# Optimization experiments

Hardware: AMD Instinct MI355X
Metric: run time of the kernel (lower is better)

Reference implementation:

```python
import jax, jax.numpy as jnp
import numpy as np

EPS = 1e-7


def setup_inputs() -> dict:
    key = jax.random.key(0)
    kx, kw, kv, kp = jax.random.split(key, 4)
    B, H, Wd, d, V, O = 4, 64, 64, 64, 64, 64
    X = jax.random.normal(kx, (B, H, Wd, d), dtype=jnp.float32)
    W = jax.random.normal(kw, (d, V), dtype=jnp.float32)
    # positive variances (kmeans-style init in original); avoid near-zero divisors
    variance = jax.random.uniform(kv, (d, V), dtype=jnp.float32) + 0.5
    weight = jax.random.normal(kp, (d, O), dtype=jnp.float32) * (1.0 / np.sqrt(d))
    return {"X": X, "W": W, "variance": variance, "weight": weight}


def reference(X, W, variance, weight):
    B, H, Wd, d = X.shape
    V = W.shape[1]
    HW = H * Wd
    Xf = X.reshape(B, HW, d)
    # Faithful replication of torch code: extend = tile(X, V) over last axis,
    # then reshape (d*V) -> (d, V) with k = a*V + c, so the X component at
    # grid position (a, c) is X[..., (a*V + c) % d].
    idx = (jnp.arange(d)[:, None] * V + jnp.arange(V)[None, :]) % d  # (d, V)
    Xg = Xf[:, :, idx]                      # (B, HW, d, V)
    q1 = (Xg - W) / variance                # (B, HW, d, V), broadcast (d,V)
    q = jnp.sum(q1 * q1, axis=2)            # (B, HW, V) squared Mahalanobis-ish dist
    q = q - jnp.min(q, axis=-1, keepdims=True)
    Q = jnp.exp(-0.5 * q)
    Q = Q / jnp.sum(Q, axis=-1, keepdims=True)          # soft assignment (B, HW, V)
    # Raw row-major reinterpretation (B, HW, d*V) -> (B, d, HW, V), as in torch
    z = q1.reshape(B, d, HW, V)
    zQ = z * Q[:, None, :, :]                            # (B, d, HW, V)
    z = jnp.sum(zQ, axis=2)                              # (B, d, V)
    Qsum = jnp.sum(Q, axis=1)                            # (B, V)
    z = (z + EPS) / (Qsum[:, None, :] + EPS)
    norm = jnp.sum(z * z, axis=1, keepdims=True)         # (B, 1, V)
    Z = z / norm                                          # (B, d, V)
    Adj = jnp.einsum('bdv,bdu->bvu', Z, Z)               # (B, V, V)
    out = jnp.einsum('bdv,do->bvo', Z, weight)           # (B, V, O)
    out = jnp.einsum('bvu,buo->bvo', Adj, out)           # (B, V, O)
    Zo = jax.nn.relu(out)
    Xn = jnp.einsum('bnv,bvo->bno', Q, Zo)               # (B, HW, O)
    return Xn.reshape(B, H, Wd, -1).transpose(0, 3, 1, 2)  # (B, O, H, W)
```

## Files before the change

### kernel.cpp

```cpp
#include <hip/hip_runtime.h>

#define HW 4096
#define EPSF 1e-7f

#define WS_S1  0
#define WS_S2P 16384
#define WS_QSP 32768
#define WS_Z   49152
#define WS_ZO  65536
#define WS_Q   81920

__global__ __launch_bounds__(512) void kA(const float* __restrict__ X,
                                          const float* __restrict__ Wm,
                                          const float* __restrict__ var,
                                          float* __restrict__ ws) {
    int b = blockIdx.x >> 6, l = blockIdx.x & 63;
    int w8 = threadIdx.x >> 6, j = threadIdx.x & 63;
    __shared__ float red[3][8][64];
    __shared__ float abc[3][64];
    float invr[8], wivr[8];
    float a = 0.f, bq = 0.f, c = 0.f;
#pragma unroll
    for (int k = 0; k < 8; k++) {
        int i = w8 * 8 + k;
        float v  = var[i * 64 + j];
        float wv = Wm[i * 64 + j];
        float iv = 1.0f / v;
        invr[k] = iv; wivr[k] = wv * iv;
        float iv2 = iv * iv;
        a += iv2; bq += wv * iv2; c += wv * wv * iv2;
    }
    red[0][w8][j] = a; red[1][w8][j] = bq; red[2][w8][j] = c;
    __syncthreads();
    if (threadIdx.x < 64) {
        float t0 = 0.f, t1 = 0.f, t2 = 0.f;
#pragma unroll
        for (int t = 0; t < 8; t++) { t0 += red[0][t][j]; t1 += red[1][t][j]; t2 += red[2][t][j]; }
        abc[0][j] = t0; abc[1][j] = t1; abc[2][j] = t2;
    }
    __syncthreads();
    float Aj = abc[0][j], Bj = abc[1][j], Cj = abc[2][j];

    float s1 = 0.f, s2 = 0.f, qsum = 0.f;
#pragma unroll
    for (int k = 0; k < 8; k++) {
        int i = w8 * 8 + k;
        int n = l * 64 + i;
        float x = X[((b * HW) + n) * 64 + j];
        float q = fmaf(fmaf(Aj, x, -2.0f * Bj), x, Cj);
        float m = q;
        for (int off = 1; off < 64; off <<= 1) m = fminf(m, __shfl_xor(m, off));
        float e = __expf(-0.5f * (q - m));
        float s = e;
        for (int off = 1; off < 64; off <<= 1) s += __shfl_xor(s, off);
        float Qv = e / s;
        ws[WS_Q + ((size_t)(b * HW) + n) * 64 + j] = Qv;
        s1 = fmaf(invr[k], Qv, s1);
        s2 = fmaf(wivr[k], Qv, s2);
        qsum += Qv;
    }
    __syncthreads();
    red[0][w8][j] = s1; red[1][w8][j] = s2; red[2][w8][j] = qsum;
    __syncthreads();
    if (threadIdx.x < 64) {
        float t0 = 0.f, t1 = 0.f, t2 = 0.f;
#pragma unroll
        for (int t = 0; t < 8; t++) { t0 += red[0][t][j]; t1 += red[1][t][j]; t2 += red[2][t][j]; }
        int idx = (b * 64 + l) * 64 + j;
        ws[WS_S1  + idx] = t0;
        ws[WS_S2P + idx] = t1;
        ws[WS_QSP + idx] = t2;
    }
}

__global__ __launch_bounds__(512) void kB(const float* __restrict__ X,
                                          float* __restrict__ ws) {
    int b = blockIdx.x >> 6, h = blockIdx.x & 63;
    int w8 = threadIdx.x >> 6, j = threadIdx.x & 63;
    float acc = 0.f, ps2 = 0.f, pqs = 0.f;
#pragma unroll
    for (int k = 0; k < 8; k++) {
        int l = w8 * 8 + k;
        float x = X[((size_t)(b * HW) + h * 64 + l) * 64 + j];
        int idx = (b * 64 + l) * 64 + j;
        acc = fmaf(x, ws[WS_S1 + idx], acc);
        ps2 += ws[WS_S2P + idx];
        pqs += ws[WS_QSP + idx];
    }
    __shared__ float ra[8][64], rb[8][64], rc[8][64];
    ra[w8][j] = acc; rb[w8][j] = ps2; rc[w8][j] = pqs;
    __syncthreads();
    if (threadIdx.x < 64) {
        float a = 0.f, s2 = 0.f, qs = 0.f;
#pragma unroll
        for (int t = 0; t < 8; t++) { a += ra[t][j]; s2 += rb[t][j]; qs += rc[t][j]; }
        ws[WS_Z + (b * 64 + h) * 64 + j] = (a - s2 + EPSF) / (qs + EPSF);
    }
}

__global__ __launch_bounds__(512) void kCD(const float* __restrict__ weight,
                                           float* __restrict__ ws) {
    int b = blockIdx.x >> 6, v = blockIdx.x & 63;
    int w8 = threadIdx.x >> 6, j = threadIdx.x & 63;
    __shared__ float zl[64][65];
    __shared__ float wl[64][65];
    __shared__ float red[8][64];
    __shared__ float sN[64], sin2[64], ghat[64], yv[64];
#pragma unroll
    for (int k = 0; k < 8; k++) {
        int idx = threadIdx.x + 512 * k;
        int r = idx >> 6, cc = idx & 63;
        zl[r][cc] = ws[WS_Z + b * 4096 + idx];
        wl[r][cc] = weight[idx];
    }
    __syncthreads();
    {
        float na = 0.f;
#pragma unroll
        for (int k = 0; k < 8; k++) { float zz = zl[w8 * 8 + k][j]; na = fmaf(zz, zz, na); }
        red[w8][j] = na;
        __syncthreads();
        if (threadIdx.x < 64) {
            float s = 0.f;
#pragma unroll
            for (int t = 0; t < 8; t++) s += red[t][j];
            sN[j] = s; sin2[j] = 1.0f / (s * s);
        }
        __syncthreads();
    }
    {
        float g = 0.f;
#pragma unroll
        for (int k = 0; k < 8; k++) { int d = w8 * 8 + k; g = fmaf(zl[d][v], zl[d][j], g); }
        red[w8][j] = g;
        __syncthreads();
        if (threadIdx.x < 64) {
            float s = 0.f;
#pragma unroll
            for (int t = 0; t < 8; t++) s += red[t][j];
            ghat[j] = s * sin2[j];
        }
        __syncthreads();
    }
    {
        float y = 0.f;
#pragma unroll
        for (int k = 0; k < 8; k++) { int u = w8 * 8 + k; y = fmaf(ghat[u], zl[j][u], y); }
        red[w8][j] = y;
        __syncthreads();
        if (threadIdx.x < 64) {
            float s = 0.f;
#pragma unroll
            for (int t = 0; t < 8; t++) s += red[t][j];
            yv[j] = s;
        }
        __syncthreads();
    }
    {
        float a = 0.f;
#pragma unroll
        for (int k = 0; k < 8; k++) { int d = w8 * 8 + k; a = fmaf(yv[d], wl[d][j], a); }
        red[w8][j] = a;
        __syncthreads();
        if (threadIdx.x < 64) {
            float s = 0.f;
#pragma unroll
            for (int t = 0; t < 8; t++) s += red[t][j];
            float r = s / sN[v];
            r = r > 0.f ? r : 0.f;
            ws[WS_ZO + (b * 64 + v) * 64 + j] = r;
        }
    }
}

__global__ __launch_bounds__(512) void kF(const float* __restrict__ ws,
                                          float* __restrict__ out) {
    int b = blockIdx.x >> 6, tb = blockIdx.x & 63;
    int nbase = tb * 64;
    int w8 = threadIdx.x >> 6, lane = threadIdx.x & 63;
    int o8 = w8 * 8;
    __shared__ float qs[64][65];
    __shared__ float zo[64][68];
#pragma unroll
    for (int k = 0; k < 8; k++) {
        int idx = threadIdx.x + 512 * k;
        int r = idx >> 6, cc = idx & 63;
        qs[r][cc] = ws[WS_Q + ((size_t)(b * HW) + nbase + r) * 64 + cc];
        zo[r][cc] = ws[WS_ZO + b * 4096 + idx];
    }
    __syncthreads();
    float acc[8];
#pragma unroll
    for (int k = 0; k < 8; k++) acc[k] = 0.f;
#pragma unroll
    for (int v = 0; v < 64; v++) {
        float qv = qs[lane][v];
        float4 z0 = *(const float4*)&zo[v][o8];
        float4 z1 = *(const float4*)&zo[v][o8 + 4];
        acc[0] = fmaf(qv, z0.x, acc[0]);
        acc[1] = fmaf(qv, z0.y, acc[1]);
        acc[2] = fmaf(qv, z0.z, acc[2]);
        acc[3] = fmaf(qv, z0.w, acc[3]);
        acc[4] = fmaf(qv, z1.x, acc[4]);
        acc[5] = fmaf(qv, z1.y, acc[5]);
        acc[6] = fmaf(qv, z1.z, acc[6]);
        acc[7] = fmaf(qv, z1.w, acc[7]);
    }
#pragma unroll
    for (int k = 0; k < 8; k++) {
        int o = o8 + k;
        out[(size_t)(b * 64 + o) * HW + nbase + lane] = acc[k];
    }
}

extern "C" void kernel_launch(void* const* d_in, const int* in_sizes, int n_in,
                              void* d_out, int out_size, void* d_ws, size_t ws_size,
                              hipStream_t stream) {
    const float* X      = (const float*)d_in[0];
    const float* Wm     = (const float*)d_in[1];
    const float* var    = (const float*)d_in[2];
    const float* weight = (const float*)d_in[3];
    float* ws  = (float*)d_ws;
    float* out = (float*)d_out;

    kA <<<256, 512, 0, stream>>>(X, Wm, var, ws);
    kB <<<256, 512, 0, stream>>>(X, ws);
    kCD<<<256, 512, 0, stream>>>(weight, ws);
    kF <<<256, 512, 0, stream>>>(ws, out);
}
```

Measured before the change: 21.51 us.

## Fuse graph-conv stage into final projection kernel with redundant per-block recompute

Merges the kCD kernel, which computes the normalized Z, adjacency, weight product and ReLU, into the final Q·Zo kernel. Each of the 64 blocks per batch now recomputes the full 64x64 Zo matrix in shared memory, with each wavefront handling 8 output rows. This removes one kernel launch and the Zo round trip through global memory. In exchange every block does 64 times the small-matmul work, and the per-wave loops are serial 64-long dot products that read shared memory.

```diff
diff --git a/kernel.cpp b/kernel.cpp
--- a/kernel.cpp
+++ b/kernel.cpp
@@ -7,8 +7,7 @@
 #define WS_S2P 16384
 #define WS_QSP 32768
 #define WS_Z   49152
-#define WS_ZO  65536
-#define WS_Q   81920
+#define WS_Q   65536
 
 __global__ __launch_bounds__(512) void kA(const float* __restrict__ X,
                                           const float* __restrict__ Wm,
@@ -98,14 +97,19 @@
     }
 }
 
-__global__ __launch_bounds__(512) void kCD(const float* __restrict__ weight,
-                                           float* __restrict__ ws) {
-    int b = blockIdx.x >> 6, v = blockIdx.x & 63;
+__global__ __launch_bounds__(512) void kFZ(const float* __restrict__ ws,
+                                           const float* __restrict__ weight,
+                                           float* __restrict__ out) {
+    int b = blockIdx.x >> 6, tb = blockIdx.x & 63;
+    int nbase = tb * 64;
     int w8 = threadIdx.x >> 6, j = threadIdx.x & 63;
+    int o8 = w8 * 8;
     __shared__ float zl[64][65];
     __shared__ float wl[64][65];
-    __shared__ float red[8][64];
-    __shared__ float sN[64], sin2[64], ghat[64], yv[64];
+    __shared__ float zo[64][68];
+    __shared__ float ghl[8][64];
+    __shared__ float yl[8][64];
+
 #pragma unroll
     for (int k = 0; k < 8; k++) {
         int idx = threadIdx.x + 512 * k;
@@ -114,87 +118,46 @@
         wl[r][cc] = weight[idx];
     }
     __syncthreads();
-    {
-        float na = 0.f;
+
+    float Nj = 0.f;
+#pragma unroll 16
+    for (int d = 0; d < 64; d++) { float zz = zl[d][j]; Nj = fmaf(zz, zz, Nj); }
+    float sin2j = 1.0f / (Nj * Nj);
+
 #pragma unroll
-        for (int k = 0; k < 8; k++) { float zz = zl[w8 * 8 + k][j]; na = fmaf(zz, zz, na); }
-        red[w8][j] = na;
-        __syncthreads();
-        if (threadIdx.x < 64) {
-            float s = 0.f;
-#pragma unroll
-            for (int t = 0; t < 8; t++) s += red[t][j];
-            sN[j] = s; sin2[j] = 1.0f / (s * s);
-        }
-        __syncthreads();
+    for (int kk = 0; kk < 8; kk++) {
+        int v = o8 + kk;
+        float g = 0.f;
+#pragma unroll 16
+        for (int d = 0; d < 64; d++) g = fmaf(zl[d][v], zl[d][j], g);
+        ghl[w8][j] = g * sin2j;
+        float y = 0.f;
+#pragma unroll 16
+        for (int u = 0; u < 64; u++) y = fmaf(ghl[w8][u], zl[j][u], y);
+        yl[w8][j] = y;
+        float a = 0.f;
+#pragma unroll 16
+        for (int d = 0; d < 64; d++) a = fmaf(yl[w8][d], wl[d][j], a);
+        float Nv = __shfl(Nj, v);
+        float r = a / Nv;
+        zo[v][j] = r > 0.f ? r : 0.f;
     }
-    {
-        float g = 0.f;
-#pragma unroll
-        for (int k = 0; k < 8; k++) { int d = w8 * 8 + k; g = fmaf(zl[d][v], zl[d][j], g); }
-        red[w8][j] = g;
-        __syncthreads();
-        if (threadIdx.x < 64) {
-            float s = 0.f;
-#pragma unroll
-            for (int t = 0; t < 8; t++) s += red[t][j];
-            ghat[j] = s * sin2[j];
-        }
-        __syncthreads();
-    }
-    {
-        float y = 0.f;
-#pragma unroll
-        for (int k = 0; k < 8; k++) { int u = w8 * 8 + k; y = fmaf(ghat[u], zl[j][u], y); }
-        red[w8][j] = y;
-        __syncthreads();
-        if (threadIdx.x < 64) {
-            float s = 0.f;
-#pragma unroll
-            for (int t = 0; t < 8; t++) s += red[t][j];
-            yv[j] = s;
-        }
-        __syncthreads();
-    }
-    {
-        float a = 0.f;
-#pragma unroll
-        for (int k = 0; k < 8; k++) { int d = w8 * 8 + k; a = fmaf(yv[d], wl[d][j], a); }
-        red[w8][j] = a;
-        __syncthreads();
-        if (threadIdx.x < 64) {
-            float s = 0.f;
-#pragma unroll
-            for (int t = 0; t < 8; t++) s += red[t][j];
-            float r = s / sN[v];
-            r = r > 0.f ? r : 0.f;
-            ws[WS_ZO + (b * 64 + v) * 64 + j] = r;
-        }
-    }
-}
+    __syncthreads();
 
-__global__ __launch_bounds__(512) void kF(const float* __restrict__ ws,
-                                          float* __restrict__ out) {
-    int b = blockIdx.x >> 6, tb = blockIdx.x & 63;
-    int nbase = tb * 64;
-    int w8 = threadIdx.x >> 6, lane = threadIdx.x & 63;
-    int o8 = w8 * 8;
-    __shared__ float qs[64][65];
-    __shared__ float zo[64][68];
 #pragma unroll
     for (int k = 0; k < 8; k++) {
         int idx = threadIdx.x + 512 * k;
         int r = idx >> 6, cc = idx & 63;
-        qs[r][cc] = ws[WS_Q + ((size_t)(b * HW) + nbase + r) * 64 + cc];
-        zo[r][cc] = ws[WS_ZO + b * 4096 + idx];
+        zl[r][cc] = ws[WS_Q + ((size_t)(b * HW) + nbase + r) * 64 + cc];
     }
     __syncthreads();
+
     float acc[8];
 #pragma unroll
     for (int k = 0; k < 8; k++) acc[k] = 0.f;
 #pragma unroll
     for (int v = 0; v < 64; v++) {
-        float qv = qs[lane][v];
+        float qv = zl[j][v];
         float4 z0 = *(const float4*)&zo[v][o8];
         float4 z1 = *(const float4*)&zo[v][o8 + 4];
         acc[0] = fmaf(qv, z0.x, acc[0]);
@@ -209,7 +172,7 @@
 #pragma unroll
     for (int k = 0; k < 8; k++) {
         int o = o8 + k;
-        out[(size_t)(b * 64 + o) * HW + nbase + lane] = acc[k];
+        out[(size_t)(b * 64 + o) * HW + nbase + j] = acc[k];
     }
 }
 
@@ -225,6 +188,5 @@
 
     kA <<<256, 512, 0, stream>>>(X, Wm, var, ws);
     kB <<<256, 512, 0, stream>>>(X, ws);
-    kCD<<<256, 512, 0, stream>>>(weight, ws);
-    kF <<<256, 512, 0, stream>>>(ws, out);
+    kFZ<<<256, 512, 0, stream>>>(ws, weight, out);
 }
```

New measurement: 39.25 us. 1.82x slower.

## Fuse four kernels into one persistent kernel with per-batch grid barriers

Applied to the files above, without the earlier changes.

Merges the four stage kernels into a single launch of 256 blocks, using per-batch atomic counters as inter-block barriers in place of kernel boundaries. Q and the X tile stay in shared memory across stages, so the global Q buffer write and read, plus the second X read, go away. The aim is to remove launch gaps and intermediate global traffic. In exchange it adds a memset launch, spin-wait barriers that assume all 256 blocks are co-resident (deadlock risk otherwise), and a larger shared-memory footprint per block.

```diff
diff --git a/kernel.cpp b/kernel.cpp
--- a/kernel.cpp
+++ b/kernel.cpp
@@ -8,208 +8,227 @@
 #define WS_QSP 32768
 #define WS_Z   49152
 #define WS_ZO  65536
-#define WS_Q   81920
-
-__global__ __launch_bounds__(512) void kA(const float* __restrict__ X,
-                                          const float* __restrict__ Wm,
-                                          const float* __restrict__ var,
-                                          float* __restrict__ ws) {
-    int b = blockIdx.x >> 6, l = blockIdx.x & 63;
-    int w8 = threadIdx.x >> 6, j = threadIdx.x & 63;
-    __shared__ float red[3][8][64];
-    __shared__ float abc[3][64];
-    float invr[8], wivr[8];
-    float a = 0.f, bq = 0.f, c = 0.f;
-#pragma unroll
-    for (int k = 0; k < 8; k++) {
-        int i = w8 * 8 + k;
-        float v  = var[i * 64 + j];
-        float wv = Wm[i * 64 + j];
-        float iv = 1.0f / v;
-        invr[k] = iv; wivr[k] = wv * iv;
-        float iv2 = iv * iv;
-        a += iv2; bq += wv * iv2; c += wv * wv * iv2;
-    }
-    red[0][w8][j] = a; red[1][w8][j] = bq; red[2][w8][j] = c;
+#define WS_CTR 81920
+
+struct __align__(16) SM {
+    float qs[64][65];
+    union __align__(16) {
+        float xt[64][65];
+        struct { float zl[64][65]; float wl[64][65]; } cd;
+        float zo[64][68];
+    } u;
+    float red[3][8][64];
+    float abc[3][64];
+    float sN[64], sin2[64], ghat[64], yv[64];
+};
+
+__device__ __forceinline__ void batch_barrier(int* ctr) {
     __syncthreads();
-    if (threadIdx.x < 64) {
-        float t0 = 0.f, t1 = 0.f, t2 = 0.f;
-#pragma unroll
-        for (int t = 0; t < 8; t++) { t0 += red[0][t][j]; t1 += red[1][t][j]; t2 += red[2][t][j]; }
-        abc[0][j] = t0; abc[1][j] = t1; abc[2][j] = t2;
+    if (threadIdx.x == 0) {
+        __threadfence();
+        __hip_atomic_fetch_add(ctr, 1, __ATOMIC_RELEASE, __HIP_MEMORY_SCOPE_AGENT);
+        while (__hip_atomic_load(ctr, __ATOMIC_ACQUIRE, __HIP_MEMORY_SCOPE_AGENT) < 64) {
+            __builtin_amdgcn_s_sleep(2);
+        }
+        __threadfence();
     }
     __syncthreads();
-    float Aj = abc[0][j], Bj = abc[1][j], Cj = abc[2][j];
-
-    float s1 = 0.f, s2 = 0.f, qsum = 0.f;
-#pragma unroll
-    for (int k = 0; k < 8; k++) {
-        int i = w8 * 8 + k;
-        int n = l * 64 + i;
-        float x = X[((b * HW) + n) * 64 + j];
-        float q = fmaf(fmaf(Aj, x, -2.0f * Bj), x, Cj);
-        float m = q;
-        for (int off = 1; off < 64; off <<= 1) m = fminf(m, __shfl_xor(m, off));
-        float e = __expf(-0.5f * (q - m));
-        float s = e;
-        for (int off = 1; off < 64; off <<= 1) s += __shfl_xor(s, off);
-        float Qv = e / s;
-        ws[WS_Q + ((size_t)(b * HW) + n) * 64 + j] = Qv;
-        s1 = fmaf(invr[k], Qv, s1);
-        s2 = fmaf(wivr[k], Qv, s2);
-        qsum += Qv;
-    }
-    __syncthreads();
-    red[0][w8][j] = s1; red[1][w8][j] = s2; red[2][w8][j] = qsum;
-    __syncthreads();
-    if (threadIdx.x < 64) {
-        float t0 = 0.f, t1 = 0.f, t2 = 0.f;
-#pragma unroll
-        for (int t = 0; t < 8; t++) { t0 += red[0][t][j]; t1 += red[1][t][j]; t2 += red[2][t][j]; }
-        int idx = (b * 64 + l) * 64 + j;
-        ws[WS_S1  + idx] = t0;
-        ws[WS_S2P + idx] = t1;
-        ws[WS_QSP + idx] = t2;
-    }
 }
 
-__global__ __launch_bounds__(512) void kB(const float* __restrict__ X,
-                                          float* __restrict__ ws) {
-    int b = blockIdx.x >> 6, h = blockIdx.x & 63;
-    int w8 = threadIdx.x >> 6, j = threadIdx.x & 63;
-    float acc = 0.f, ps2 = 0.f, pqs = 0.f;
-#pragma unroll
-    for (int k = 0; k < 8; k++) {
-        int l = w8 * 8 + k;
-        float x = X[((size_t)(b * HW) + h * 64 + l) * 64 + j];
-        int idx = (b * 64 + l) * 64 + j;
-        acc = fmaf(x, ws[WS_S1 + idx], acc);
-        ps2 += ws[WS_S2P + idx];
-        pqs += ws[WS_QSP + idx];
-    }
-    __shared__ float ra[8][64], rb[8][64], rc[8][64];
-    ra[w8][j] = acc; rb[w8][j] = ps2; rc[w8][j] = pqs;
-    __syncthreads();
-    if (threadIdx.x < 64) {
-        float a = 0.f, s2 = 0.f, qs = 0.f;
-#pragma unroll
-        for (int t = 0; t < 8; t++) { a += ra[t][j]; s2 += rb[t][j]; qs += rc[t][j]; }
-        ws[WS_Z + (b * 64 + h) * 64 + j] = (a - s2 + EPSF) / (qs + EPSF);
-    }
-}
-
-__global__ __launch_bounds__(512) void kCD(const float* __restrict__ weight,
-                                           float* __restrict__ ws) {
-    int b = blockIdx.x >> 6, v = blockIdx.x & 63;
-    int w8 = threadIdx.x >> 6, j = threadIdx.x & 63;
-    __shared__ float zl[64][65];
-    __shared__ float wl[64][65];
-    __shared__ float red[8][64];
-    __shared__ float sN[64], sin2[64], ghat[64], yv[64];
-#pragma unroll
-    for (int k = 0; k < 8; k++) {
-        int idx = threadIdx.x + 512 * k;
-        int r = idx >> 6, cc = idx & 63;
-        zl[r][cc] = ws[WS_Z + b * 4096 + idx];
-        wl[r][cc] = weight[idx];
-    }
-    __syncthreads();
-    {
-        float na = 0.f;
-#pragma unroll
-        for (int k = 0; k < 8; k++) { float zz = zl[w8 * 8 + k][j]; na = fmaf(zz, zz, na); }
-        red[w8][j] = na;
-        __syncthreads();
-        if (threadIdx.x < 64) {
-            float s = 0.f;
-#pragma unroll
-            for (int t = 0; t < 8; t++) s += red[t][j];
-            sN[j] = s; sin2[j] = 1.0f / (s * s);
-        }
-        __syncthreads();
-    }
-    {
-        float g = 0.f;
-#pragma unroll
-        for (int k = 0; k < 8; k++) { int d = w8 * 8 + k; g = fmaf(zl[d][v], zl[d][j], g); }
-        red[w8][j] = g;
-        __syncthreads();
-        if (threadIdx.x < 64) {
-            float s = 0.f;
-#pragma unroll
-            for (int t = 0; t < 8; t++) s += red[t][j];
-            ghat[j] = s * sin2[j];
-        }
-        __syncthreads();
-    }
-    {
-        float y = 0.f;
-#pragma unroll
-        for (int k = 0; k < 8; k++) { int u = w8 * 8 + k; y = fmaf(ghat[u], zl[j][u], y); }
-        red[w8][j] = y;
-        __syncthreads();
-        if (threadIdx.x < 64) {
-            float s = 0.f;
-#pragma unroll
-            for (int t = 0; t < 8; t++) s += red[t][j];
-            yv[j] = s;
-        }
-        __syncthreads();
-    }
-    {
-        float a = 0.f;
-#pragma unroll
-        for (int k = 0; k < 8; k++) { int d = w8 * 8 + k; a = fmaf(yv[d], wl[d][j], a); }
-        red[w8][j] = a;
-        __syncthreads();
-        if (threadIdx.x < 64) {
-            float s = 0.f;
-#pragma unroll
-            for (int t = 0; t < 8; t++) s += red[t][j];
-            float r = s / sN[v];
-            r = r > 0.f ? r : 0.f;
-            ws[WS_ZO + (b * 64 + v) * 64 + j] = r;
-        }
-    }
-}
-
-__global__ __launch_bounds__(512) void kF(const float* __restrict__ ws,
-                                          float* __restrict__ out) {
-    int b = blockIdx.x >> 6, tb = blockIdx.x & 63;
-    int nbase = tb * 64;
-    int w8 = threadIdx.x >> 6, lane = threadIdx.x & 63;
-    int o8 = w8 * 8;
-    __shared__ float qs[64][65];
-    __shared__ float zo[64][68];
-#pragma unroll
-    for (int k = 0; k < 8; k++) {
-        int idx = threadIdx.x + 512 * k;
-        int r = idx >> 6, cc = idx & 63;
-        qs[r][cc] = ws[WS_Q + ((size_t)(b * HW) + nbase + r) * 64 + cc];
-        zo[r][cc] = ws[WS_ZO + b * 4096 + idx];
-    }
-    __syncthreads();
-    float acc[8];
-#pragma unroll
-    for (int k = 0; k < 8; k++) acc[k] = 0.f;
-#pragma unroll
-    for (int v = 0; v < 64; v++) {
-        float qv = qs[lane][v];
-        float4 z0 = *(const float4*)&zo[v][o8];
-        float4 z1 = *(const float4*)&zo[v][o8 + 4];
-        acc[0] = fmaf(qv, z0.x, acc[0]);
-        acc[1] = fmaf(qv, z0.y, acc[1]);
-        acc[2] = fmaf(qv, z0.z, acc[2]);
-        acc[3] = fmaf(qv, z0.w, acc[3]);
-        acc[4] = fmaf(qv, z1.x, acc[4]);
-        acc[5] = fmaf(qv, z1.y, acc[5]);
-        acc[6] = fmaf(qv, z1.z, acc[6]);
-        acc[7] = fmaf(qv, z1.w, acc[7]);
-    }
-#pragma unroll
-    for (int k = 0; k < 8; k++) {
-        int o = o8 + k;
-        out[(size_t)(b * 64 + o) * HW + nbase + lane] = acc[k];
+__global__ __launch_bounds__(512) void fused(const float* __restrict__ X,
+                                             const float* __restrict__ Wm,
+                                             const float* __restrict__ var,
+                                             const float* __restrict__ weight,
+                                             float* __restrict__ ws,
+                                             float* __restrict__ out) {
+    __shared__ SM sm;
+    const int b = blockIdx.x >> 6, s = blockIdx.x & 63;
+    const int t = threadIdx.x;
+    const int w8 = t >> 6, j = t & 63;
+    int* ctr  = (int*)(ws + WS_CTR);
+    int* ctrA = ctr + b;
+    int* ctrB = ctr + 4 + b;
+    int* ctrC = ctr + 8 + b;
+
+    {
+        float invr[8], wivr[8];
+        float a = 0.f, bq = 0.f, c = 0.f;
+#pragma unroll
+        for (int k = 0; k < 8; k++) {
+            int i = w8 * 8 + k;
+            float v  = var[i * 64 + j];
+            float wv = Wm[i * 64 + j];
+            float iv = 1.0f / v;
+            invr[k] = iv; wivr[k] = wv * iv;
+            float iv2 = iv * iv;
+            a += iv2; bq += wv * iv2; c += wv * wv * iv2;
+        }
+        sm.red[0][w8][j] = a; sm.red[1][w8][j] = bq; sm.red[2][w8][j] = c;
+        __syncthreads();
+        if (t < 64) {
+            float t0 = 0.f, t1 = 0.f, t2 = 0.f;
+#pragma unroll
+            for (int w = 0; w < 8; w++) { t0 += sm.red[0][w][j]; t1 += sm.red[1][w][j]; t2 += sm.red[2][w][j]; }
+            sm.abc[0][j] = t0; sm.abc[1][j] = t1; sm.abc[2][j] = t2;
+        }
+        __syncthreads();
+        float Aj = sm.abc[0][j], Bj = sm.abc[1][j], Cj = sm.abc[2][j];
+
+        float s1 = 0.f, s2 = 0.f, qsum = 0.f;
+#pragma unroll
+        for (int k = 0; k < 8; k++) {
+            int i = w8 * 8 + k;
+            int n = s * 64 + i;
+            float x = X[((size_t)(b * HW) + n) * 64 + j];
+            sm.u.xt[i][j] = x;
+            float q = fmaf(fmaf(Aj, x, -2.0f * Bj), x, Cj);
+            float m = q;
+            for (int off = 1; off < 64; off <<= 1) m = fminf(m, __shfl_xor(m, off));
+            float e = __expf(-0.5f * (q - m));
+            float sum = e;
+            for (int off = 1; off < 64; off <<= 1) sum += __shfl_xor(sum, off);
+            float Qv = e / sum;
+            sm.qs[i][j] = Qv;
+            s1 = fmaf(invr[k], Qv, s1);
+            s2 = fmaf(wivr[k], Qv, s2);
+            qsum += Qv;
+        }
+        __syncthreads();
+        sm.red[0][w8][j] = s1; sm.red[1][w8][j] = s2; sm.red[2][w8][j] = qsum;
+        __syncthreads();
+        if (t < 64) {
+            float t0 = 0.f, t1 = 0.f, t2 = 0.f;
+#pragma unroll
+            for (int w = 0; w < 8; w++) { t0 += sm.red[0][w][j]; t1 += sm.red[1][w][j]; t2 += sm.red[2][w][j]; }
+            int idx = (b * 64 + s) * 64 + j;
+            ws[WS_S1  + idx] = t0;
+            ws[WS_S2P + idx] = t1;
+            ws[WS_QSP + idx] = t2;
+        }
+    }
+    batch_barrier(ctrA);
+
+    {
+        float acc = 0.f, ps2 = 0.f, pqs = 0.f;
+#pragma unroll
+        for (int k = 0; k < 8; k++) {
+            int l = w8 * 8 + k;
+            int idx = (b * 64 + l) * 64 + j;
+            acc = fmaf(sm.u.xt[l][j], ws[WS_S1 + idx], acc);
+            ps2 += ws[WS_S2P + idx];
+            pqs += ws[WS_QSP + idx];
+        }
+        __syncthreads();
+        sm.red[0][w8][j] = acc; sm.red[1][w8][j] = ps2; sm.red[2][w8][j] = pqs;
+        __syncthreads();
+        if (t < 64) {
+            float a = 0.f, s2 = 0.f, qs = 0.f;
+#pragma unroll
+            for (int w = 0; w < 8; w++) { a += sm.red[0][w][j]; s2 += sm.red[1][w][j]; qs += sm.red[2][w][j]; }
+            ws[WS_Z + (b * 64 + s) * 64 + j] = (a - s2 + EPSF) / (qs + EPSF);
+        }
+    }
+    batch_barrier(ctrB);
+
+    {
+#pragma unroll
+        for (int k = 0; k < 8; k++) {
+            int idx = t + 512 * k;
+            int r = idx >> 6, cc = idx & 63;
+            sm.u.cd.zl[r][cc] = ws[WS_Z + b * 4096 + idx];
+            sm.u.cd.wl[r][cc] = weight[idx];
+        }
+        __syncthreads();
+        {
+            float na = 0.f;
+#pragma unroll
+            for (int k = 0; k < 8; k++) { float zz = sm.u.cd.zl[w8 * 8 + k][j]; na = fmaf(zz, zz, na); }
+            sm.red[0][w8][j] = na;
+            __syncthreads();
+            if (t < 64) {
+                float acc = 0.f;
+#pragma unroll
+                for (int w = 0; w < 8; w++) acc += sm.red[0][w][j];
+                sm.sN[j] = acc; sm.sin2[j] = 1.0f / (acc * acc);
+            }
+            __syncthreads();
+        }
+        {
+            float g = 0.f;
+#pragma unroll
+            for (int k = 0; k < 8; k++) { int d = w8 * 8 + k; g = fmaf(sm.u.cd.zl[d][s], sm.u.cd.zl[d][j], g); }
+            sm.red[0][w8][j] = g;
+            __syncthreads();
+            if (t < 64) {
+                float acc = 0.f;
+#pragma unroll
+                for (int w = 0; w < 8; w++) acc += sm.red[0][w][j];
+                sm.ghat[j] = acc * sm.sin2[j];
+            }
+            __syncthreads();
+        }
+        {
+            float y = 0.f;
+#pragma unroll
+            for (int k = 0; k < 8; k++) { int u = w8 * 8 + k; y = fmaf(sm.ghat[u], sm.u.cd.zl[j][u], y); }
+            sm.red[0][w8][j] = y;
+            __syncthreads();
+            if (t < 64) {
+                float acc = 0.f;
+#pragma unroll
+                for (int w = 0; w < 8; w++) acc += sm.red[0][w][j];
+                sm.yv[j] = acc;
+            }
+            __syncthreads();
+        }
+        {
+            float a = 0.f;
+#pragma unroll
+            for (int k = 0; k < 8; k++) { int d = w8 * 8 + k; a = fmaf(sm.yv[d], sm.u.cd.wl[d][j], a); }
+            sm.red[0][w8][j] = a;
+            __syncthreads();
+            if (t < 64) {
+                float acc = 0.f;
+#pragma unroll
+                for (int w = 0; w < 8; w++) acc += sm.red[0][w][j];
+                float r = acc / sm.sN[s];
+                r = r > 0.f ? r : 0.f;
+                ws[WS_ZO + (b * 64 + s) * 64 + j] = r;
+            }
+        }
+    }
+    batch_barrier(ctrC);
+
+    {
+        int o8 = w8 * 8;
+#pragma unroll
+        for (int k = 0; k < 8; k++) {
+            int idx = t + 512 * k;
+            sm.u.zo[idx >> 6][idx & 63] = ws[WS_ZO + b * 4096 + idx];
+        }
+        __syncthreads();
+        float acc[8];
+#pragma unroll
+        for (int k = 0; k < 8; k++) acc[k] = 0.f;
+#pragma unroll
+        for (int v = 0; v < 64; v++) {
+            float qv = sm.qs[j][v];
+            float4 z0 = *(const float4*)&sm.u.zo[v][o8];
+            float4 z1 = *(const float4*)&sm.u.zo[v][o8 + 4];
+            acc[0] = fmaf(qv, z0.x, acc[0]);
+            acc[1] = fmaf(qv, z0.y, acc[1]);
+            acc[2] = fmaf(qv, z0.z, acc[2]);
+            acc[3] = fmaf(qv, z0.w, acc[3]);
+            acc[4] = fmaf(qv, z1.x, acc[4]);
+            acc[5] = fmaf(qv, z1.y, acc[5]);
+            acc[6] = fmaf(qv, z1.z, acc[6]);
+            acc[7] = fmaf(qv, z1.w, acc[7]);
+        }
+#pragma unroll
+        for (int k = 0; k < 8; k++) {
+            int o = o8 + k;
+            out[(size_t)(b * 64 + o) * HW + s * 64 + j] = acc[k];
+        }
     }
 }
 
@@ -223,8 +242,6 @@
     float* ws  = (float*)d_ws;
     float* out = (float*)d_out;
 
-    kA <<<256, 512, 0, stream>>>(X, Wm, var, ws);
-    kB <<<256, 512, 0, stream>>>(X, ws);
-    kCD<<<256, 512, 0, stream>>>(weight, ws);
-    kF <<<256, 512, 0, stream>>>(ws, out);
+    hipMemsetAsync((char*)d_ws + WS_CTR * sizeof(float), 0, 12 * sizeof(int), stream);
+    fused<<<256, 512, 0, stream>>>(X, Wm, var, weight, ws, out);
 }
```

Result: slower. 85.29 us (+296.5%).
